# Kernel tuning notes

Hardware: AMD Instinct MI355X
Metric: run time of the kernel (lower is better)

## Reference

```python
import jax, jax.numpy as jnp
import numpy as np

B, T, C = 4, 2048, 2048
H, D, L = 16, 128, 512


def _rope(x, cos, sin):
    # x: [B, T, H, D]; cos/sin: [T, D//2]; consecutive-pair complex rotation
    x2 = x.reshape(*x.shape[:-1], -1, 2)
    x0, x1 = x2[..., 0], x2[..., 1]
    c = cos[None, :, None, :]
    s = sin[None, :, None, :]
    o0 = x0 * c - x1 * s
    o1 = x0 * s + x1 * c
    return jnp.stack([o0, o1], axis=-1).reshape(x.shape)


def setup_inputs() -> dict:
    key = jax.random.key(0)
    ks = jax.random.split(key, 8)
    x = jax.random.normal(ks[0], (B, T, C), dtype=jnp.float32)
    # rotary table, theta = 10000
    inv_freq = 1.0 / (10000.0 ** (np.arange(0, D, 2, dtype=np.float32) / D))
    ang = np.outer(np.arange(T, dtype=np.float32), inv_freq)
    freqs_cos = jnp.asarray(np.cos(ang), dtype=jnp.float32)
    freqs_sin = jnp.asarray(np.sin(ang), dtype=jnp.float32)
    sc = 0.02
    wq = sc * jax.random.normal(ks[1], (H * D, C), dtype=jnp.float32)
    wkv_down = sc * jax.random.normal(ks[2], (L, C), dtype=jnp.float32)
    wk_up = sc * jax.random.normal(ks[3], (D, L), dtype=jnp.float32)
    wv_up = sc * jax.random.normal(ks[4], (D, L), dtype=jnp.float32)
    wo = sc * jax.random.normal(ks[5], (C, H * D), dtype=jnp.float32)
    return {"x": x, "freqs_cos": freqs_cos, "freqs_sin": freqs_sin,
            "wq": wq, "wkv_down": wkv_down, "wk_up": wk_up,
            "wv_up": wv_up, "wo": wo}


def reference(x, freqs_cos, freqs_sin, wq, wkv_down, wk_up, wv_up, wo):
    Bc, Tc, Cc = x.shape
    # query projection -> [B, T, H, D]
    q = jnp.einsum('btc,ec->bte', x, wq).reshape(Bc, Tc, H, D)
    # shared latent KV: [B, T, L]
    kv_latent = jnp.einsum('btc,lc->btl', x, wkv_down)
    # up-project to single shared head: [B, T, D]
    k = jnp.einsum('btl,dl->btd', kv_latent, wk_up)
    v = jnp.einsum('btl,dl->btd', kv_latent, wv_up)
    # RoPE on q (per head) and k (single shared head)
    q = _rope(q, freqs_cos, freqs_sin)
    k = _rope(k[:, :, None, :], freqs_cos, freqs_sin)[:, :, 0, :]
    # causal SDPA; k/v are shared across heads (MLA) so avoid expanding them
    scale = 1.0 / jnp.sqrt(jnp.asarray(D, dtype=x.dtype))
    scores = jnp.einsum('bthd,bsd->bhts', q, k) * scale  # [B, H, T, S]
    causal = jnp.tril(jnp.ones((Tc, Tc), dtype=bool))
    scores = jnp.where(causal[None, None, :, :], scores, jnp.finfo(x.dtype).min)
    probs = jax.nn.softmax(scores, axis=-1)
    y = jnp.einsum('bhts,bsd->bthd', probs, v).reshape(Bc, Tc, H * D)
    return jnp.einsum('bte,ce->btc', y, wo)
```

## Files before the change

### kernel.cpp

```cpp
#include <hip/hip_runtime.h>
#include <hip/hip_bf16.h>
#include <cstddef>

#define BB 4
#define TT 2048
#define CC 2048
#define HH 16
#define DD 128
#define LL 512

typedef _Float16 f16;
typedef f16 f16x2 __attribute__((ext_vector_type(2)));
typedef f16 f16x4 __attribute__((ext_vector_type(4)));
typedef f16 f16x8 __attribute__((ext_vector_type(8)));
typedef float f32x4 __attribute__((ext_vector_type(4)));

__device__ __forceinline__ void async_load16(void* lptr, const void* gptr) {
  __builtin_amdgcn_global_load_lds(
      (const __attribute__((address_space(1))) unsigned int*)gptr,
      (__attribute__((address_space(3))) unsigned int*)lptr, 16, 0, 0);
}

template <int EPI>
__global__ __launch_bounds__(512, 2) void mla_gemm_256(
    const f16* __restrict__ A, const f16* __restrict__ B,
    void* __restrict__ Cv, int M, int N, int K,
    const float* __restrict__ cosb, const float* __restrict__ sinb) {
  __shared__ __align__(16) f16 smem[2][2][256 * 64];

  const int tid = threadIdx.x;
  const int lane = tid & 63;
  const int w = tid >> 6;
  const int lnm = lane & 15, quad = lane >> 4;
  const int wm = w >> 2, wn = w & 3;

  const int nwg = gridDim.x;
  const int bid0 = blockIdx.x;
  const int q8 = nwg >> 3, r8 = nwg & 7;
  const int xcd = bid0 & 7, lid = bid0 >> 3;
  const int wg =
      (xcd < r8 ? xcd * (q8 + 1) : r8 * (q8 + 1) + (xcd - r8) * q8) + lid;
  const int ntc = N >> 8;
  const int m0 = (wg / ntc) * 256;
  const int n0 = (wg % ntc) * 256;

  const int srow = tid >> 3;
  const int sch = (tid & 7) ^ ((tid >> 3) & 7);
  const f16* Ag = A + (size_t)(m0 + srow) * K + sch * 8;
  const f16* Bg = B + (size_t)(n0 + srow) * K + sch * 8;

  auto stage = [&](int bi, int k0, int h) {
    const int mat = h >> 1;
    const int rb = (h & 1) * 128;
    const f16* g = (mat ? Bg : Ag) + (size_t)rb * K + k0;
    f16* l = &smem[bi][mat][rb * 64 + tid * 8];
    async_load16(l, g);
    async_load16(l + 4096, g + (size_t)64 * K);
  };

  const int rx8 = lnm & 7;
  auto rdA = [&](const f16* Ab, int i, int ks) -> f16x8 {
    return *(const f16x8*)&Ab[(wm * 128 + i * 16 + lnm) * 64 +
                              (((ks * 4 + quad) ^ rx8) * 8)];
  };
  auto rdB = [&](const f16* Bb, int j, int ks) -> f16x8 {
    return *(const f16x8*)&Bb[(wn * 64 + j * 16 + lnm) * 64 +
                              (((ks * 4 + quad) ^ rx8) * 8)];
  };

  f32x4 acc[8][4] = {};

  const int NT = K >> 6;

  stage(0, 0, 0);
  stage(0, 0, 1);
  stage(0, 0, 2);
  stage(0, 0, 3);
  stage(1, 64, 0);
  asm volatile("s_waitcnt vmcnt(2)" ::: "memory");
  __builtin_amdgcn_s_barrier();

  for (int t = 0; t < NT; ++t) {
    const int bi = t & 1;
    const f16* Ab = smem[bi][0];
    const f16* Bb = smem[bi][1];
    const int k1 = (t + 1 < NT ? t + 1 : t) << 6;
    const int k2 = (t + 2 < NT ? t + 2 : t) << 6;

    f16x8 Ar[4][2], Br[2][2];

#pragma unroll
    for (int i = 0; i < 4; i++)
#pragma unroll
      for (int ks = 0; ks < 2; ks++) Ar[i][ks] = rdA(Ab, i, ks);
#pragma unroll
    for (int j = 0; j < 2; j++)
#pragma unroll
      for (int ks = 0; ks < 2; ks++) Br[j][ks] = rdB(Bb, j, ks);
    stage(bi ^ 1, k1, 1);
    __builtin_amdgcn_s_barrier();
    asm volatile("s_waitcnt lgkmcnt(0)" ::: "memory");
    __builtin_amdgcn_s_setprio(1);
#pragma unroll
    for (int i = 0; i < 4; i++)
#pragma unroll
      for (int j = 0; j < 2; j++)
#pragma unroll
        for (int ks = 0; ks < 2; ks++)
          acc[i][j] = __builtin_amdgcn_mfma_f32_16x16x32_f16(
              Ar[i][ks], Br[j][ks], acc[i][j], 0, 0, 0);
    __builtin_amdgcn_s_setprio(0);
    __builtin_amdgcn_s_barrier();

#pragma unroll
    for (int j = 0; j < 2; j++)
#pragma unroll
      for (int ks = 0; ks < 2; ks++) Br[j][ks] = rdB(Bb, 2 + j, ks);
    stage(bi ^ 1, k1, 2);
    __builtin_amdgcn_s_barrier();
    asm volatile("s_waitcnt lgkmcnt(0)" ::: "memory");
    __builtin_amdgcn_s_setprio(1);
#pragma unroll
    for (int i = 0; i < 4; i++)
#pragma unroll
      for (int j = 0; j < 2; j++)
#pragma unroll
        for (int ks = 0; ks < 2; ks++)
          acc[i][2 + j] = __builtin_amdgcn_mfma_f32_16x16x32_f16(
              Ar[i][ks], Br[j][ks], acc[i][2 + j], 0, 0, 0);
    __builtin_amdgcn_s_setprio(0);
    __builtin_amdgcn_s_barrier();

#pragma unroll
    for (int i = 0; i < 4; i++)
#pragma unroll
      for (int ks = 0; ks < 2; ks++) Ar[i][ks] = rdA(Ab, 4 + i, ks);
    stage(bi ^ 1, k1, 3);
    __builtin_amdgcn_s_barrier();
    asm volatile("s_waitcnt lgkmcnt(0)" ::: "memory");
    __builtin_amdgcn_s_setprio(1);
#pragma unroll
    for (int i = 0; i < 4; i++)
#pragma unroll
      for (int j = 0; j < 2; j++)
#pragma unroll
        for (int ks = 0; ks < 2; ks++)
          acc[4 + i][2 + j] = __builtin_amdgcn_mfma_f32_16x16x32_f16(
              Ar[i][ks], Br[j][ks], acc[4 + i][2 + j], 0, 0, 0);
    __builtin_amdgcn_s_setprio(0);
    __builtin_amdgcn_s_barrier();

#pragma unroll
    for (int j = 0; j < 2; j++)
#pragma unroll
      for (int ks = 0; ks < 2; ks++) Br[j][ks] = rdB(Bb, j, ks);
    stage(bi, k2, 0);
    __builtin_amdgcn_s_barrier();
    asm volatile("s_waitcnt lgkmcnt(0)" ::: "memory");
    __builtin_amdgcn_s_setprio(1);
#pragma unroll
    for (int i = 0; i < 4; i++)
#pragma unroll
      for (int j = 0; j < 2; j++)
#pragma unroll
        for (int ks = 0; ks < 2; ks++)
          acc[4 + i][j] = __builtin_amdgcn_mfma_f32_16x16x32_f16(
              Ar[i][ks], Br[j][ks], acc[4 + i][j], 0, 0, 0);
    __builtin_amdgcn_s_setprio(0);
    asm volatile("s_waitcnt vmcnt(2)" ::: "memory");
    __builtin_amdgcn_s_barrier();
  }

  asm volatile("s_waitcnt vmcnt(0)" ::: "memory");

  if constexpr (EPI == 0) {
    float* C = (float*)Cv;
#pragma unroll
    for (int i = 0; i < 8; i++)
#pragma unroll
      for (int r = 0; r < 4; r++) {
        float* crow = C + (size_t)(m0 + wm * 128 + i * 16 + quad * 4 + r) * N +
                      n0 + wn * 64 + lnm;
#pragma unroll
        for (int j = 0; j < 4; j++) crow[j * 16] = acc[i][j][r];
      }
  } else {
    f16* C = (f16*)Cv;
    const float SCLQ = 0.1275174280f;
#pragma unroll
    for (int i = 0; i < 8; i++)
#pragma unroll
      for (int r = 0; r < 4; r++) {
        const int m = m0 + wm * 128 + i * 16 + quad * 4 + r;
        const int t = m & (TT - 1);
#pragma unroll
        for (int j = 0; j < 4; j++) {
          const int col = n0 + wn * 64 + j * 16 + lnm;
          float v = acc[i][j][r];
          float u = __shfl_xor(v, 1, 64);
          const int fi = (col & (DD - 1)) >> 1;
          const float ct = cosb[t * (DD / 2) + fi];
          const float st2 = sinb[t * (DD / 2) + fi];
          const float o =
              (lnm & 1) ? (u * st2 + v * ct) : (v * ct - u * st2);
          C[(size_t)m * N + col] = (f16)(o * SCLQ);
        }
      }
  }
}

__global__ __launch_bounds__(256) void mla_gemm_mfma(
    const f16* __restrict__ A, const f16* __restrict__ B,
    float* __restrict__ C, int M, int N, int K) {
  __shared__ f16 As[128 * 32];
  __shared__ f16 Bs[128 * 32];

  const int tid = threadIdx.x;
  const int lane = tid & 63;
  const int w = tid >> 6;
  const int lnm = lane & 15, quad = lane >> 4;
  const int wm = w >> 1, wn = w & 1;
  const int m0 = blockIdx.y * 128;
  const int n0 = blockIdx.x * 128;

  const int srow = tid >> 2;
  const int skoff = (tid & 3) * 8;

  f32x4 acc[4][4] = {};

  for (int k0 = 0; k0 < K; k0 += 32) {
    const f16* ag = A + (size_t)(m0 + srow) * K + k0 + skoff;
    const f16* bg = B + (size_t)(n0 + srow) * K + k0 + skoff;
    async_load16(&As[(size_t)tid * 8], ag);
    async_load16(&As[(size_t)(256 + tid) * 8], ag + (size_t)64 * K);
    async_load16(&Bs[(size_t)tid * 8], bg);
    async_load16(&Bs[(size_t)(256 + tid) * 8], bg + (size_t)64 * K);
    __syncthreads();

    f16x8 af[4], bf[4];
#pragma unroll
    for (int i = 0; i < 4; i++)
      af[i] = *(const f16x8*)&As[(wm * 64 + i * 16 + lnm) * 32 + quad * 8];
#pragma unroll
    for (int j = 0; j < 4; j++)
      bf[j] = *(const f16x8*)&Bs[(wn * 64 + j * 16 + lnm) * 32 + quad * 8];
#pragma unroll
    for (int i = 0; i < 4; i++)
#pragma unroll
      for (int j = 0; j < 4; j++)
        acc[i][j] = __builtin_amdgcn_mfma_f32_16x16x32_f16(af[i], bf[j],
                                                           acc[i][j], 0, 0, 0);
    __syncthreads();
  }

#pragma unroll
  for (int i = 0; i < 4; i++)
#pragma unroll
    for (int r = 0; r < 4; r++) {
      float* crow = C + (size_t)(m0 + wm * 64 + i * 16 + quad * 4 + r) * N +
                    n0 + wn * 64 + lnm;
#pragma unroll
      for (int j = 0; j < 4; j++) crow[j * 16] = acc[i][j][r];
    }
}

__global__ __launch_bounds__(256) void mla_cvt_f16(
    const float4* __restrict__ in, f16* __restrict__ out, int n4) {
  int i = blockIdx.x * 256 + threadIdx.x;
  if (i >= n4) return;
  float4 v = in[i];
  f16x4 r = {(f16)v.x, (f16)v.y, (f16)v.z, (f16)v.w};
  *(f16x4*)(out + (size_t)i * 4) = r;
}

__global__ __launch_bounds__(256) void mla_rope_k(
    const float2* __restrict__ x, f16* __restrict__ khp,
    const float* __restrict__ cosb, const float* __restrict__ sinb,
    int ld2, int total) {
  int idx = blockIdx.x * blockDim.x + threadIdx.x;
  if (idx >= total) return;
  const int i = idx & 63;
  const int m = idx >> 6;
  const int t = m & (TT - 1);
  const int b = m >> 11;
  float c = cosb[t * 64 + i];
  float s = sinb[t * 64 + i];
  float2 v = x[(size_t)m * ld2 + i];
  f16x2 r;
  r.x = (f16)(v.x * c - v.y * s);
  r.y = (f16)(v.x * s + v.y * c);
  const int st = t >> 6, sl = t & 63;
  const int cq = i >> 2, e = (i & 3) * 2;
  size_t off = (((size_t)(b * 32 + st) * 16 + cq) * 64 + sl) * 8 + e;
  *(f16x2*)(khp + off) = r;
}

__global__ __launch_bounds__(256) void mla_fragv(
    const float* __restrict__ v, f16* __restrict__ vtp, int ldv) {
  __shared__ f16 tl[64][128];
  const int b = blockIdx.z;
  const int st = blockIdx.x;
  const int t = threadIdx.x;

  const int dl = (t & 31) * 4;
#pragma unroll
  for (int r = 0; r < 8; r++) {
    const int s = r * 8 + (t >> 5);
    float4 val = *(const float4*)&v[((size_t)(b * TT + st * 64 + s)) * ldv + dl];
    f16x4 h = {(f16)val.x, (f16)val.y, (f16)val.z, (f16)val.w};
    *(f16x4*)&tl[s][dl] = h;
  }
  __syncthreads();

  f16* outb = vtp + (size_t)(b * 32 + st) * 8192;
#pragma unroll
  for (int k = 0; k < 4; k++) {
    const int cd = k * 256 + t;
    const int cq2 = cd >> 7, d = cd & 127;
    const int c = cq2 >> 2, quad = cq2 & 3;
    f16x8 o;
#pragma unroll
    for (int e = 0; e < 8; e++) {
      const int s = c * 32 + quad * 4 + ((e >> 2) << 4) + (e & 3);
      o[e] = tl[s][d];
    }
    *(f16x8*)&outb[(size_t)cd * 8] = o;
  }
}

__global__ __launch_bounds__(512, 2) void mla_flash2(
    const f16* __restrict__ qh, const f16* __restrict__ khp,
    const f16* __restrict__ vtp, f16* __restrict__ y) {
  __shared__ __align__(16) f16 Ks[2][8192];
  __shared__ __align__(16) f16 Vs[2][8192];

  const int tid = threadIdx.x;
  const int lane = tid & 63;
  const int w = tid >> 6;
  const int lnm = lane & 15, quad = lane >> 4;

  const int bid = blockIdx.x;
  const int qt = (TT / 256 - 1) - (bid >> 6);
  const int bh = bid & 63;
  const int b = bh >> 4, h = bh & 15;
  const int q0b = qt * 256;
  const int q0 = q0b + w * 32;

  f16x8 qf[2][4];
#pragma unroll
  for (int qnb = 0; qnb < 2; qnb++) {
    const f16* qrow =
        qh + ((size_t)(b * TT + q0 + qnb * 16 + lnm) * HH + h) * DD;
#pragma unroll
    for (int c = 0; c < 4; c++)
      qf[qnb][c] = *(const f16x8*)(qrow + c * 32 + quad * 8);
  }

  f32x4 O[2][8] = {};
  float l_acc[2] = {0.f, 0.f};

  const int nst = (q0b + 256) / 64;
  const int wmax = q0 + 31;
  const f16* kpb = khp + (size_t)b * 32 * 8192;
  const f16* vpb = vtp + (size_t)b * 32 * 8192;

  auto stageK = [&](int buf, int st) {
    const f16* g = kpb + (size_t)st * 8192 + (size_t)tid * 8;
    async_load16(&Ks[buf][(size_t)tid * 8], g);
    async_load16(&Ks[buf][(size_t)(512 + tid) * 8], g + 4096);
  };
  auto stageV = [&](int buf, int st) {
    const f16* g = vpb + (size_t)st * 8192 + (size_t)tid * 8;
    async_load16(&Vs[buf][(size_t)tid * 8], g);
    async_load16(&Vs[buf][(size_t)(512 + tid) * 8], g + 4096);
  };

  const int kbo = quad * 512 + lnm * 8;
  const int vbo = quad * 1024 + lnm * 8;

  stageK(0, 0);
  stageV(0, 0);
  __syncthreads();

  for (int st = 0; st < nst; st++) {
    const int cur = st & 1;
    const int s0 = st * 64;
    if (st + 1 < nst) {
      stageK(cur ^ 1, st + 1);
      stageV(cur ^ 1, st + 1);
    }

    if (s0 <= wmax) {
      const f16* kl = &Ks[cur][kbo];
      const f16* vl = &Vs[cur][vbo];

      f32x4 S[2][4] = {};
      __builtin_amdgcn_s_setprio(1);
#pragma unroll
      for (int sb = 0; sb < 4; sb++)
#pragma unroll
        for (int c = 0; c < 4; c++) {
          f16x8 ka = *(const f16x8*)&kl[c * 2048 + sb * 128];
          S[0][sb] = __builtin_amdgcn_mfma_f32_16x16x32_f16(ka, qf[0][c],
                                                            S[0][sb], 0, 0, 0);
          S[1][sb] = __builtin_amdgcn_mfma_f32_16x16x32_f16(ka, qf[1][c],
                                                            S[1][sb], 0, 0, 0);
        }
      __builtin_amdgcn_s_setprio(0);

      f16x8 P8[2][2];
      const bool domask = (s0 + 63 > q0);
      if (!domask) {
#pragma unroll
        for (int qnb = 0; qnb < 2; qnb++) {
          float lp = 0.f;
#pragma unroll
          for (int sb = 0; sb < 4; sb++)
#pragma unroll
            for (int j = 0; j < 4; j++) {
              float p = __builtin_amdgcn_exp2f(S[qnb][sb][j]);
              lp += p;
              P8[qnb][sb >> 1][(sb & 1) * 4 + j] = (f16)p;
            }
          l_acc[qnb] += lp;
        }
      } else {
#pragma unroll
        for (int qnb = 0; qnb < 2; qnb++) {
          const int m_abs = q0 + qnb * 16 + lnm;
          float lp = 0.f;
#pragma unroll
          for (int sb = 0; sb < 4; sb++) {
            const int srow = s0 + sb * 16 + quad * 4;
#pragma unroll
            for (int j = 0; j < 4; j++) {
              float p = __builtin_amdgcn_exp2f(S[qnb][sb][j]);
              if (srow + j > m_abs) p = 0.f;
              lp += p;
              P8[qnb][sb >> 1][(sb & 1) * 4 + j] = (f16)p;
            }
          }
          l_acc[qnb] += lp;
        }
      }

      __builtin_amdgcn_s_setprio(1);
#pragma unroll
      for (int c = 0; c < 2; c++)
#pragma unroll
        for (int db = 0; db < 8; db++) {
          f16x8 vb = *(const f16x8*)&vl[c * 4096 + db * 128];
          O[0][db] = __builtin_amdgcn_mfma_f32_16x16x32_f16(P8[0][c], vb,
                                                            O[0][db], 0, 0, 0);
          O[1][db] = __builtin_amdgcn_mfma_f32_16x16x32_f16(P8[1][c], vb,
                                                            O[1][db], 0, 0, 0);
        }
      __builtin_amdgcn_s_setprio(0);
    }
    __syncthreads();
  }

#pragma unroll
  for (int qnb = 0; qnb < 2; qnb++) {
    float l = l_acc[qnb];
    l += __shfl_xor(l, 16, 64);
    l += __shfl_xor(l, 32, 64);
    l_acc[qnb] = l;
  }

#pragma unroll
  for (int qnb = 0; qnb < 2; qnb++) {
    float linv[4];
#pragma unroll
    for (int r = 0; r < 4; r++)
      linv[r] = 1.f / __shfl(l_acc[qnb], quad * 4 + r, 64);
#pragma unroll
    for (int db = 0; db < 8; db++)
#pragma unroll
      for (int r = 0; r < 4; r++) {
        size_t off =
            ((size_t)(b * TT + q0 + qnb * 16 + quad * 4 + r) * HH + h) * DD +
            db * 16 + lnm;
        y[off] = (f16)(O[qnb][db][r] * linv[r]);
      }
  }
}

extern "C" void kernel_launch(void* const* d_in, const int* in_sizes, int n_in,
                              void* d_out, int out_size, void* d_ws,
                              size_t ws_size, hipStream_t stream) {
  const float* x      = (const float*)d_in[0];
  const float* fcos   = (const float*)d_in[1];
  const float* fsin   = (const float*)d_in[2];
  const float* wq     = (const float*)d_in[3];
  const float* wkv_dn = (const float*)d_in[4];
  const float* wk_up  = (const float*)d_in[5];
  const float* wv_up  = (const float*)d_in[6];
  const float* wo     = (const float*)d_in[7];
  float* out = (float*)d_out;

  const int M = BB * TT;

  float* ws = (float*)d_ws;
  float* qbuf   = ws;
  float* kv     = qbuf + (size_t)M * CC;
  float* kkvv   = kv + (size_t)M * LL;
  f16*   xh     = (f16*)(kkvv + (size_t)M * 256);
  f16*   wqh    = xh + (size_t)M * CC;
  f16*   wdownh = wqh + (size_t)CC * CC;
  f16*   wkvuph = wdownh + (size_t)LL * CC;
  f16*   woh    = wkvuph + (size_t)256 * LL;
  f16*   kvh    = woh + (size_t)CC * CC;
  f16*   khp    = kvh + (size_t)M * LL;
  f16*   vtp    = khp + (size_t)M * DD;
  f16*   qh     = (f16*)qbuf;
  f16*   yh     = qh + (size_t)M * CC;

  dim3 blk(256);

  mla_cvt_f16<<<(M * CC / 4 + 255) / 256, blk, 0, stream>>>(
      (const float4*)x, xh, M * CC / 4);
  mla_cvt_f16<<<(CC * CC / 4 + 255) / 256, blk, 0, stream>>>(
      (const float4*)wq, wqh, CC * CC / 4);
  mla_cvt_f16<<<(LL * CC / 4 + 255) / 256, blk, 0, stream>>>(
      (const float4*)wkv_dn, wdownh, LL * CC / 4);
  mla_cvt_f16<<<(DD * LL / 4 + 255) / 256, blk, 0, stream>>>(
      (const float4*)wk_up, wkvuph, DD * LL / 4);
  mla_cvt_f16<<<(DD * LL / 4 + 255) / 256, blk, 0, stream>>>(
      (const float4*)wv_up, wkvuph + (size_t)DD * LL, DD * LL / 4);
  mla_cvt_f16<<<(CC * CC / 4 + 255) / 256, blk, 0, stream>>>(
      (const float4*)wo, woh, CC * CC / 4);

  mla_gemm_256<1><<<dim3((M / 256) * (CC / 256)), dim3(512), 0, stream>>>(
      xh, wqh, qh, M, CC, CC, fcos, fsin);
  mla_gemm_mfma<<<dim3(LL / 128, M / 128), blk, 0, stream>>>(
      xh, wdownh, kv, M, LL, CC);

  mla_cvt_f16<<<(M * LL / 4 + 255) / 256, blk, 0, stream>>>(
      (const float4*)kv, kvh, M * LL / 4);
  mla_gemm_mfma<<<dim3(256 / 128, M / 128), blk, 0, stream>>>(
      kvh, wkvuph, kkvv, M, 256, LL);

  {
    int total_k = BB * TT * (DD / 2);
    mla_rope_k<<<(total_k + 255) / 256, blk, 0, stream>>>(
        (const float2*)kkvv, khp, fcos, fsin, 128, total_k);
  }

  mla_fragv<<<dim3(TT / 64, 1, BB), blk, 0, stream>>>(kkvv + 128, vtp, 256);

  mla_flash2<<<dim3(BB * HH * (TT / 256)), dim3(512), 0, stream>>>(
      qh, khp, vtp, yh);

  mla_gemm_256<0><<<dim3((M / 256) * (CC / 256)), dim3(512), 0, stream>>>(
      yh, woh, out, M, CC, CC, nullptr, nullptr);
}
```

Baseline: 454.8 us.

## Fuse conversions, KV epilogues with RoPE/layout, and software-pipeline QK in flash kernel

Replaces six fp32-to-fp16 conversion launches with a single combined conversion kernel. The down-projection GEMM now writes fp16 directly, and the up-projection GEMM applies RoPE to K and writes the fragment-packed K and V layouts in its epilogue. This removes the intermediate fp32 buffers and the separate rope and transpose kernels. In the flash attention kernel, the QK^T for the next tile is computed before the PV for the current one, with K staged two tiles ahead. That overlaps MFMA work with the softmax, at the cost of more registers and a more intricate buffer rotation.

```diff
diff --git a/kernel.cpp b/kernel.cpp
--- a/kernel.cpp
+++ b/kernel.cpp
@@ -209,9 +209,9 @@
   }
 }
 
-__global__ __launch_bounds__(256) void mla_gemm_mfma(
+__global__ __launch_bounds__(256) void mla_gemm_mfma_h(
     const f16* __restrict__ A, const f16* __restrict__ B,
-    float* __restrict__ C, int M, int N, int K) {
+    f16* __restrict__ C, int M, int N, int K) {
   __shared__ f16 As[128 * 32];
   __shared__ f16 Bs[128 * 32];
 
@@ -257,75 +257,118 @@
   for (int i = 0; i < 4; i++)
 #pragma unroll
     for (int r = 0; r < 4; r++) {
-      float* crow = C + (size_t)(m0 + wm * 64 + i * 16 + quad * 4 + r) * N +
-                    n0 + wn * 64 + lnm;
-#pragma unroll
-      for (int j = 0; j < 4; j++) crow[j * 16] = acc[i][j][r];
+      f16* crow = C + (size_t)(m0 + wm * 64 + i * 16 + quad * 4 + r) * N +
+                  n0 + wn * 64 + lnm;
+#pragma unroll
+      for (int j = 0; j < 4; j++) crow[j * 16] = (f16)acc[i][j][r];
     }
 }
 
-__global__ __launch_bounds__(256) void mla_cvt_f16(
-    const float4* __restrict__ in, f16* __restrict__ out, int n4) {
-  int i = blockIdx.x * 256 + threadIdx.x;
-  if (i >= n4) return;
-  float4 v = in[i];
+__global__ __launch_bounds__(256) void mla_gemm_upkv(
+    const f16* __restrict__ A, const f16* __restrict__ B,
+    f16* __restrict__ khp, f16* __restrict__ vtp,
+    const float* __restrict__ cosb, const float* __restrict__ sinb) {
+  const int NN = 256, KK = 512;
+  __shared__ f16 As[128 * 32];
+  __shared__ f16 Bs[128 * 32];
+
+  const int tid = threadIdx.x;
+  const int lane = tid & 63;
+  const int w = tid >> 6;
+  const int lnm = lane & 15, quad = lane >> 4;
+  const int wm = w >> 1, wn = w & 1;
+  const int m0 = blockIdx.y * 128;
+  const int n0 = blockIdx.x * 128;
+
+  const int srow = tid >> 2;
+  const int skoff = (tid & 3) * 8;
+
+  f32x4 acc[4][4] = {};
+
+  for (int k0 = 0; k0 < KK; k0 += 32) {
+    const f16* ag = A + (size_t)(m0 + srow) * KK + k0 + skoff;
+    const f16* bg = B + (size_t)(n0 + srow) * KK + k0 + skoff;
+    async_load16(&As[(size_t)tid * 8], ag);
+    async_load16(&As[(size_t)(256 + tid) * 8], ag + (size_t)64 * KK);
+    async_load16(&Bs[(size_t)tid * 8], bg);
+    async_load16(&Bs[(size_t)(256 + tid) * 8], bg + (size_t)64 * KK);
+    __syncthreads();
+
+    f16x8 af[4], bf[4];
+#pragma unroll
+    for (int i = 0; i < 4; i++)
+      af[i] = *(const f16x8*)&As[(wm * 64 + i * 16 + lnm) * 32 + quad * 8];
+#pragma unroll
+    for (int j = 0; j < 4; j++)
+      bf[j] = *(const f16x8*)&Bs[(wn * 64 + j * 16 + lnm) * 32 + quad * 8];
+#pragma unroll
+    for (int i = 0; i < 4; i++)
+#pragma unroll
+      for (int j = 0; j < 4; j++)
+        acc[i][j] = __builtin_amdgcn_mfma_f32_16x16x32_f16(af[i], bf[j],
+                                                           acc[i][j], 0, 0, 0);
+    __syncthreads();
+  }
+
+  const bool isv = (n0 != 0);
+#pragma unroll
+  for (int i = 0; i < 4; i++)
+#pragma unroll
+    for (int r = 0; r < 4; r++) {
+      const int m = m0 + wm * 64 + i * 16 + quad * 4 + r;
+      const int b = m >> 11, t = m & (TT - 1);
+      const int st = t >> 6, s = t & 63;
+      if (!isv) {
+        f16* tb = khp + (size_t)(b * 32 + st) * 8192;
+#pragma unroll
+        for (int j = 0; j < 4; j++) {
+          const int n = wn * 64 + j * 16 + lnm;
+          float v = acc[i][j][r];
+          float u = __shfl_xor(v, 1, 64);
+          const int fi = n >> 1;
+          const float ct = cosb[t * 64 + fi];
+          const float st2 = sinb[t * 64 + fi];
+          const float o = (lnm & 1) ? (u * st2 + v * ct) : (v * ct - u * st2);
+          tb[(n >> 3) * 512 + s * 8 + (n & 7)] = (f16)o;
+        }
+      } else {
+        const int cq2 = ((s >> 5) << 2) | ((s >> 2) & 3);
+        const int e = (((s >> 4) & 1) << 2) | (s & 3);
+        f16* tb = vtp + (size_t)(b * 32 + st) * 8192 + cq2 * 1024 + e;
+#pragma unroll
+        for (int j = 0; j < 4; j++) {
+          const int d = wn * 64 + j * 16 + lnm;
+          tb[d * 8] = (f16)acc[i][j][r];
+        }
+      }
+    }
+}
+
+#define CVT_C0 ((size_t)BB * TT * CC)
+#define CVT_C1 (CVT_C0 + (size_t)CC * CC)
+#define CVT_C2 (CVT_C1 + (size_t)LL * CC)
+#define CVT_C3 (CVT_C2 + (size_t)DD * LL)
+#define CVT_C4 (CVT_C3 + (size_t)DD * LL)
+#define CVT_C5 (CVT_C4 + (size_t)CC * CC)
+__global__ __launch_bounds__(256) void mla_cvt_all(
+    const float* __restrict__ x, const float* __restrict__ wq,
+    const float* __restrict__ wdn, const float* __restrict__ wku,
+    const float* __restrict__ wvu, const float* __restrict__ wo,
+    f16* __restrict__ dst) {
+  size_t i4 = (size_t)blockIdx.x * 256 + threadIdx.x;
+  if (i4 >= CVT_C5 / 4) return;
+  size_t e = i4 * 4;
+  const float* src;
+  size_t off;
+  if (e < CVT_C0) { src = x; off = e; }
+  else if (e < CVT_C1) { src = wq; off = e - CVT_C0; }
+  else if (e < CVT_C2) { src = wdn; off = e - CVT_C1; }
+  else if (e < CVT_C3) { src = wku; off = e - CVT_C2; }
+  else if (e < CVT_C4) { src = wvu; off = e - CVT_C3; }
+  else { src = wo; off = e - CVT_C4; }
+  float4 v = *(const float4*)&src[off];
   f16x4 r = {(f16)v.x, (f16)v.y, (f16)v.z, (f16)v.w};
-  *(f16x4*)(out + (size_t)i * 4) = r;
-}
-
-__global__ __launch_bounds__(256) void mla_rope_k(
-    const float2* __restrict__ x, f16* __restrict__ khp,
-    const float* __restrict__ cosb, const float* __restrict__ sinb,
-    int ld2, int total) {
-  int idx = blockIdx.x * blockDim.x + threadIdx.x;
-  if (idx >= total) return;
-  const int i = idx & 63;
-  const int m = idx >> 6;
-  const int t = m & (TT - 1);
-  const int b = m >> 11;
-  float c = cosb[t * 64 + i];
-  float s = sinb[t * 64 + i];
-  float2 v = x[(size_t)m * ld2 + i];
-  f16x2 r;
-  r.x = (f16)(v.x * c - v.y * s);
-  r.y = (f16)(v.x * s + v.y * c);
-  const int st = t >> 6, sl = t & 63;
-  const int cq = i >> 2, e = (i & 3) * 2;
-  size_t off = (((size_t)(b * 32 + st) * 16 + cq) * 64 + sl) * 8 + e;
-  *(f16x2*)(khp + off) = r;
-}
-
-__global__ __launch_bounds__(256) void mla_fragv(
-    const float* __restrict__ v, f16* __restrict__ vtp, int ldv) {
-  __shared__ f16 tl[64][128];
-  const int b = blockIdx.z;
-  const int st = blockIdx.x;
-  const int t = threadIdx.x;
-
-  const int dl = (t & 31) * 4;
-#pragma unroll
-  for (int r = 0; r < 8; r++) {
-    const int s = r * 8 + (t >> 5);
-    float4 val = *(const float4*)&v[((size_t)(b * TT + st * 64 + s)) * ldv + dl];
-    f16x4 h = {(f16)val.x, (f16)val.y, (f16)val.z, (f16)val.w};
-    *(f16x4*)&tl[s][dl] = h;
-  }
-  __syncthreads();
-
-  f16* outb = vtp + (size_t)(b * 32 + st) * 8192;
-#pragma unroll
-  for (int k = 0; k < 4; k++) {
-    const int cd = k * 256 + t;
-    const int cq2 = cd >> 7, d = cd & 127;
-    const int c = cq2 >> 2, quad = cq2 & 3;
-    f16x8 o;
-#pragma unroll
-    for (int e = 0; e < 8; e++) {
-      const int s = c * 32 + quad * 4 + ((e >> 2) << 4) + (e & 3);
-      o[e] = tl[s][d];
-    }
-    *(f16x8*)&outb[(size_t)cd * 8] = o;
-  }
+  *(f16x4*)(dst + e) = r;
 }
 
 __global__ __launch_bounds__(512, 2) void mla_flash2(
@@ -357,6 +400,7 @@
   }
 
   f32x4 O[2][8] = {};
+  f32x4 S[2][4];
   float l_acc[2] = {0.f, 0.f};
 
   const int nst = (q0b + 256) / 64;
@@ -378,37 +422,41 @@
   const int kbo = quad * 512 + lnm * 8;
   const int vbo = quad * 1024 + lnm * 8;
 
+  auto qk = [&](const f16* Kbuf) {
+    const f16* kl = Kbuf + kbo;
+    const f32x4 z = {0.f, 0.f, 0.f, 0.f};
+#pragma unroll
+    for (int qnb = 0; qnb < 2; qnb++)
+#pragma unroll
+      for (int sb = 0; sb < 4; sb++) S[qnb][sb] = z;
+#pragma unroll
+    for (int sb = 0; sb < 4; sb++)
+#pragma unroll
+      for (int c = 0; c < 4; c++) {
+        f16x8 ka = *(const f16x8*)&kl[c * 2048 + sb * 128];
+        S[0][sb] = __builtin_amdgcn_mfma_f32_16x16x32_f16(ka, qf[0][c],
+                                                          S[0][sb], 0, 0, 0);
+        S[1][sb] = __builtin_amdgcn_mfma_f32_16x16x32_f16(ka, qf[1][c],
+                                                          S[1][sb], 0, 0, 0);
+      }
+  };
+
   stageK(0, 0);
   stageV(0, 0);
   __syncthreads();
+  stageK(1, 1);
+  qk(Ks[0]);
+  __syncthreads();
 
   for (int st = 0; st < nst; st++) {
-    const int cur = st & 1;
+    const int cur = st & 1, nxt = cur ^ 1;
     const int s0 = st * 64;
-    if (st + 1 < nst) {
-      stageK(cur ^ 1, st + 1);
-      stageV(cur ^ 1, st + 1);
-    }
-
-    if (s0 <= wmax) {
-      const f16* kl = &Ks[cur][kbo];
-      const f16* vl = &Vs[cur][vbo];
-
-      f32x4 S[2][4] = {};
-      __builtin_amdgcn_s_setprio(1);
-#pragma unroll
-      for (int sb = 0; sb < 4; sb++)
-#pragma unroll
-        for (int c = 0; c < 4; c++) {
-          f16x8 ka = *(const f16x8*)&kl[c * 2048 + sb * 128];
-          S[0][sb] = __builtin_amdgcn_mfma_f32_16x16x32_f16(ka, qf[0][c],
-                                                            S[0][sb], 0, 0, 0);
-          S[1][sb] = __builtin_amdgcn_mfma_f32_16x16x32_f16(ka, qf[1][c],
-                                                            S[1][sb], 0, 0, 0);
-        }
-      __builtin_amdgcn_s_setprio(0);
-
-      f16x8 P8[2][2];
+    stageK(cur, st + 2 < nst ? st + 2 : nst - 1);
+    stageV(nxt, st + 1 < nst ? st + 1 : nst - 1);
+
+    const bool act = (s0 <= wmax);
+    f16x8 P8[2][2];
+    if (act) {
       const bool domask = (s0 + 63 > q0);
       if (!domask) {
 #pragma unroll
@@ -443,8 +491,13 @@
           l_acc[qnb] += lp;
         }
       }
-
-      __builtin_amdgcn_s_setprio(1);
+    }
+
+    __builtin_amdgcn_s_setprio(1);
+    if ((st + 1) * 64 <= wmax) qk(Ks[nxt]);
+
+    if (act) {
+      const f16* vl = &Vs[cur][vbo];
 #pragma unroll
       for (int c = 0; c < 2; c++)
 #pragma unroll
@@ -455,8 +508,8 @@
           O[1][db] = __builtin_amdgcn_mfma_f32_16x16x32_f16(P8[1][c], vb,
                                                             O[1][db], 0, 0, 0);
         }
-      __builtin_amdgcn_s_setprio(0);
     }
+    __builtin_amdgcn_s_setprio(0);
     __syncthreads();
   }
 
@@ -503,9 +556,7 @@
 
   float* ws = (float*)d_ws;
   float* qbuf   = ws;
-  float* kv     = qbuf + (size_t)M * CC;
-  float* kkvv   = kv + (size_t)M * LL;
-  f16*   xh     = (f16*)(kkvv + (size_t)M * 256);
+  f16*   xh     = (f16*)(qbuf + (size_t)M * CC);
   f16*   wqh    = xh + (size_t)M * CC;
   f16*   wdownh = wqh + (size_t)CC * CC;
   f16*   wkvuph = wdownh + (size_t)LL * CC;
@@ -516,38 +567,20 @@
   f16*   qh     = (f16*)qbuf;
   f16*   yh     = qh + (size_t)M * CC;
 
-  dim3 blk(256);
-
-  mla_cvt_f16<<<(M * CC / 4 + 255) / 256, blk, 0, stream>>>(
-      (const float4*)x, xh, M * CC / 4);
-  mla_cvt_f16<<<(CC * CC / 4 + 255) / 256, blk, 0, stream>>>(
-      (const float4*)wq, wqh, CC * CC / 4);
-  mla_cvt_f16<<<(LL * CC / 4 + 255) / 256, blk, 0, stream>>>(
-      (const float4*)wkv_dn, wdownh, LL * CC / 4);
-  mla_cvt_f16<<<(DD * LL / 4 + 255) / 256, blk, 0, stream>>>(
-      (const float4*)wk_up, wkvuph, DD * LL / 4);
-  mla_cvt_f16<<<(DD * LL / 4 + 255) / 256, blk, 0, stream>>>(
-      (const float4*)wv_up, wkvuph + (size_t)DD * LL, DD * LL / 4);
-  mla_cvt_f16<<<(CC * CC / 4 + 255) / 256, blk, 0, stream>>>(
-      (const float4*)wo, woh, CC * CC / 4);
+  {
+    size_t total4 = CVT_C5 / 4;
+    mla_cvt_all<<<(unsigned)((total4 + 255) / 256), dim3(256), 0, stream>>>(
+        x, wq, wkv_dn, wk_up, wv_up, wo, xh);
+  }
 
   mla_gemm_256<1><<<dim3((M / 256) * (CC / 256)), dim3(512), 0, stream>>>(
       xh, wqh, qh, M, CC, CC, fcos, fsin);
-  mla_gemm_mfma<<<dim3(LL / 128, M / 128), blk, 0, stream>>>(
-      xh, wdownh, kv, M, LL, CC);
-
-  mla_cvt_f16<<<(M * LL / 4 + 255) / 256, blk, 0, stream>>>(
-      (const float4*)kv, kvh, M * LL / 4);
-  mla_gemm_mfma<<<dim3(256 / 128, M / 128), blk, 0, stream>>>(
-      kvh, wkvuph, kkvv, M, 256, LL);
-
-  {
-    int total_k = BB * TT * (DD / 2);
-    mla_rope_k<<<(total_k + 255) / 256, blk, 0, stream>>>(
-        (const float2*)kkvv, khp, fcos, fsin, 128, total_k);
-  }
-
-  mla_fragv<<<dim3(TT / 64, 1, BB), blk, 0, stream>>>(kkvv + 128, vtp, 256);
+
+  mla_gemm_mfma_h<<<dim3(LL / 128, M / 128), dim3(256), 0, stream>>>(
+      xh, wdownh, kvh, M, LL, CC);
+
+  mla_gemm_upkv<<<dim3(2, M / 128), dim3(256), 0, stream>>>(
+      kvh, wkvuph, khp, vtp, fcos, fsin);
 
   mla_flash2<<<dim3(BB * HH * (TT / 256)), dim3(512), 0, stream>>>(
       qh, khp, vtp, yh);
```

Result: faster. 432.1 us (-5.0%).
